# Kernel tuning notes

Measured on AMD Instinct MI355X. Metric: run time of the kernel, lower is better.

Reference implementation:

```python
import jax, jax.numpy as jnp
import numpy as np
import math

B, C_IN, C_OUT, H, W = 16, 128, 128, 56, 56
K, S, P, D = 3, 1, 1, 1
PROD_KS = K * K


def _unfold(x, k, s, p, d):
    # torch.nn.functional.unfold equivalent -> (B, k*k, C, Ho*Wo)
    b, c, h, w = x.shape
    ho = (h + 2 * p - d * (k - 1) - 1) // s + 1
    wo = (w + 2 * p - d * (k - 1) - 1) // s + 1
    xp = jnp.pad(x, ((0, 0), (0, 0), (p, p), (p, p)))
    patches = [
        xp[:, :, i * d: i * d + (ho - 1) * s + 1: s, j * d: j * d + (wo - 1) * s + 1: s]
        for i in range(k) for j in range(k)
    ]
    u = jnp.stack(patches, axis=1)  # (B, K2, C, Ho, Wo)
    return u.reshape(b, k * k, c, ho * wo), ho, wo


def setup_inputs() -> dict:
    key = jax.random.key(0)
    k1, k2, k3, k4 = jax.random.split(key, 4)
    stdv = 1.0 / math.sqrt(C_IN * PROD_KS)
    x = jax.random.normal(k1, (B, C_IN, H, W), dtype=jnp.float32)
    weight = jax.random.uniform(k2, (1, PROD_KS, C_OUT, C_IN), dtype=jnp.float32,
                                minval=-stdv, maxval=stdv)
    b_k = jax.random.uniform(k3, (1, PROD_KS, 1, C_OUT, 1), dtype=jnp.float32,
                             minval=-stdv, maxval=stdv)
    bias = jax.random.uniform(k4, (C_OUT,), dtype=jnp.float32, minval=-stdv, maxval=stdv)
    return {"x": x, "weight": weight, "b_k": b_k, "bias": bias}


def reference(x, weight, b_k, bias):
    batch = x.shape[0]
    u, ho, wo = _unfold(x, K, S, P, D)          # (B, K2, C_in, L)
    inpt = u.transpose(0, 1, 3, 2)               # (B, K2, L, C_in)
    # GEMM: (B,K2,L,Cin) x (K2,Cout,Cin) -> (B,K2,L,Cout)
    out = jnp.einsum('bklc,koc->bklo', inpt, weight[0])
    bk = b_k[0, :, 0, :, 0]                      # (K2, Cout)
    # fused cos/sin contraction over kernel positions -> (B, L, Cout) each
    a = jnp.einsum('bklo,ko->blo', out, jnp.cos(bk))
    bb = jnp.einsum('bklo,ko->blo', out, jnp.sin(bk))
    eps = 1e-05
    a_gt = a > 0
    b_gt = bb > 0
    ab_eq = a_gt == b_gt
    theta = jnp.where(ab_eq, jnp.arctan(bb / (a + eps)), -jnp.arctan(a / (bb + eps)))
    pi = math.pi
    peak = jnp.where(ab_eq & a_gt, pi / 2.0,
           jnp.where(ab_eq & ~a_gt, -pi / 2.0,
           jnp.where(~ab_eq & ~b_gt, -pi, 0.0)))
    theta = peak - theta
    o = jnp.sin(theta) * a + jnp.cos(theta) * bb  # (B, L, Cout)
    o = o.transpose(0, 2, 1) + bias[None, :, None]  # (B, Cout, L)
    conv_out = o.reshape(batch, C_OUT, ho, wo)
    theta_out = (theta / pi).transpose(0, 2, 1).reshape(batch, C_OUT, ho, wo)
    return jnp.concatenate([conv_out, theta_out], axis=1)
```

## Files before the change

### kernel.cpp

```cpp
#include <hip/hip_runtime.h>
#include <hip/hip_bf16.h>
#include <math.h>

#define NB   16
#define CIN  128
#define COUT 128
#define HH   56
#define WW   56
#define LL   3136

typedef __attribute__((ext_vector_type(8))) short short8;
typedef __attribute__((ext_vector_type(16))) float f32x16;
typedef __attribute__((ext_vector_type(4))) float f32x4;
typedef __attribute__((ext_vector_type(4))) unsigned int uint4v;

#define PXT    256
#define NPXT   13
#define XC     58
#define XPLANE 7424
#define XUSH   14848
#define XUNITS 1856
#define XHALF  928
#define WUSH   9216
#define WBYTES 18432
#define WUNITS 1152


#define XT_ROWS 62
#define XT_PLANE_USH (XT_ROWS*XC*16)
#define XT_CG_STRIDE 3682304

#define CSD_OFF 256
#define WSP_OFF 32768
#define XT_OFF  1212416
#define XT_SIZE 29458432
#define WL_OFF  (XT_OFF + XT_SIZE)

__global__ void prep_kernel(const float* __restrict__ w, const float* __restrict__ bk,
                            const float* __restrict__ x,
                            double* __restrict__ csd, unsigned short* __restrict__ wsp,
                            unsigned short* __restrict__ xt, unsigned* __restrict__ cnt) {
    int bid = blockIdx.x;
    if (bid == 0 && threadIdx.x == 0) *cnt = 0u;
    if (bid < 576) {
        int i = bid * 256 + threadIdx.x;
        if (i >= 9*COUT*CIN) return;
        int k = i / (COUT*CIN);
        int rem = i - k*(COUT*CIN);
        int oc = rem >> 7, c = rem & 127;
        float bkv = bk[k*COUT + oc];
        if (c == 0) {
            double bd = (double)bkv;
            csd[k*COUT + oc]          = cos(bd);
            csd[9*COUT + k*COUT + oc] = sin(bd);
        }
        float ck = cosf(bkv), sk = sinf(bkv);
        float wv = w[i];
        float fa = ck * wv;
        float fb = sk * wv;
        __hip_bfloat16 ah = __float2bfloat16(fa);
        __hip_bfloat16 al = __float2bfloat16(fa - __bfloat162float(ah));
        __hip_bfloat16 bh = __float2bfloat16(fb);
        __hip_bfloat16 bl = __float2bfloat16(fb - __bfloat162float(bh));
        int ocb = oc >> 4;
        int row_a = oc & 15;
        int cg = c >> 4, cp = c & 15;
        int lane_a = row_a + ((cp >> 3) << 5);
        int lane_b = 16 + row_a + ((cp >> 3) << 5);
        int bp = cp & 7;
        size_t img = ((size_t)ocb*8 + cg) * WUSH;
        wsp[img + (size_t)((k*2+0)*64 + lane_a)*8 + bp] = *(unsigned short*)&ah;
        wsp[img + (size_t)((k*2+0)*64 + lane_b)*8 + bp] = *(unsigned short*)&bh;
        wsp[img + (size_t)((k*2+1)*64 + lane_a)*8 + bp] = *(unsigned short*)&al;
        wsp[img + (size_t)((k*2+1)*64 + lane_b)*8 + bp] = *(unsigned short*)&bl;
    } else {
        int i = (bid - 576) * 256 + threadIdx.x;
        if (i < 100352) {
            int c4 = i % 14; int t = i / 14;
            int row1 = t % 56; t /= 56;
            int bat = t & 15, cg = t >> 4;
            const float* xp = x + ((size_t)(bat*CIN + cg*16))*LL + row1*WW + c4*4;
            unsigned short hi[4][16], lo[4][16];
            #pragma unroll
            for (int j = 0; j < 16; j++) {
                f32x4 v = *(const f32x4*)(xp + (size_t)j*LL);
                #pragma unroll
                for (int cc = 0; cc < 4; cc++) {
                    float f = v[cc];
                    __hip_bfloat16 h = __float2bfloat16(f);
                    __hip_bfloat16 l = __float2bfloat16(f - __bfloat162float(h));
                    hi[cc][j] = *(unsigned short*)&h;
                    lo[cc][j] = *(unsigned short*)&l;
                }
            }
            size_t base = ((((size_t)cg*16 + bat)*2 + 0)*XT_ROWS + (row1+1))*XC + (c4*4 + 1);
            #pragma unroll
            for (int cc = 0; cc < 4; cc++) {
                unsigned short* dh = xt + (base + cc)*16;
                unsigned short* dl = dh + XT_PLANE_USH;
                *(uint4v*)dh       = *(const uint4v*)&hi[cc][0];
                *(uint4v*)(dh + 8) = *(const uint4v*)&hi[cc][8];
                *(uint4v*)dl       = *(const uint4v*)&lo[cc][0];
                *(uint4v*)(dl + 8) = *(const uint4v*)&lo[cc][8];
            }
        } else if (i < 218112) {
            int i2 = i - 100352;
            int unit = i2 % 460; int t = i2 / 460;
            int pl = t & 1; t >>= 1;
            int bat = t & 15, cg = t >> 4;
            int row, c58;
            if (unit < 348) {
                int zr = unit / 58; c58 = unit - zr*58;
                row = (zr == 0) ? 0 : (56 + zr);
            } else {
                int u2 = unit - 348; row = 1 + (u2 >> 1); c58 = (u2 & 1) ? 57 : 0;
            }
            size_t base = ((((size_t)cg*16 + bat)*2 + pl)*XT_ROWS + row)*XC + c58;
            uint4v zz = {0u,0u,0u,0u};
            *(uint4v*)(xt + base*16)     = zz;
            *(uint4v*)(xt + base*16 + 8) = zz;
        }
    }
}

__global__ __launch_bounds__(256, 3)
void mfma_kernel(const unsigned short* __restrict__ xt, const unsigned short* __restrict__ wsp,
                 const float* __restrict__ bias, float* __restrict__ out,
                 unsigned* __restrict__ cnt, unsigned* __restrict__ wl, unsigned cap)
{
    __shared__ __align__(16) unsigned short SMX[XUSH];
    __shared__ __align__(16) unsigned short SMW[WUSH];
    __shared__ float sm_bias[16];

    const int tid = threadIdx.x;
    int bid = blockIdx.x;
    int wk = (bid & 7) * 208 + (bid >> 3);
    const int ocb = wk & 7; wk >>= 3;
    const int pxt = wk % NPXT;
    const int bat = wk / NPXT;
    const int l0  = pxt * PXT;
    const int o0  = ocb * 16;
    const int yf  = l0 / WW;

    const int lane = tid & 63;
    const int n    = lane & 31;
    const int kh   = lane >> 5;
    const int wave = tid >> 6;

    if (tid < 16) sm_bias[tid] = bias[o0 + tid];

    unsigned xoff[8];
    #pragma unroll
    for (int k = 0; k < 8; k++) {
        int u = tid + 256*k;
        int uc = u < XUNITS ? u : XUNITS-1;
        int pl = uc >= XHALF ? 1 : 0;
        int rem = uc - pl*XHALF;
        int q  = rem >> 1;
        int hl = rem & 1;
        int hg = hl ^ ((q >> 2) & 1);
        int r  = q / XC;
        int c  = q - r*XC;
        xoff[k] = (unsigned)((((bat*2 + pl)*XT_ROWS + (yf + r))*XC + c)*32 + hg*16);
    }

    int q0g[2];
    #pragma unroll
    for (int g = 0; g < 2; g++) {
        int p  = l0 + wave*64 + g*32 + n;
        int pc = p < LL ? p : LL-1;
        int py = pc / WW, pxx = pc - py*WW;
        q0g[g] = (py - yf)*XC + pxx;
    }

    f32x16 acc[2];
    #pragma unroll
    for (int g = 0; g < 2; g++) {
        #pragma unroll
        for (int r = 0; r < 16; r++) acc[g][r] = 0.f;
    }

    const char* xtB  = (const char*)xt;
    const char* wspB = (const char*)wsp + (size_t)ocb * (8*(size_t)WBYTES);

    auto stage_x = [&](int chn) {
        const char* xp = xtB + (size_t)chn * XT_CG_STRIDE;
        #pragma unroll
        for (int k = 0; k < 7; k++) {
            __builtin_amdgcn_global_load_lds(
                (const __attribute__((address_space(1))) unsigned int*)(xp + xoff[k]),
                (__attribute__((address_space(3))) unsigned int*)&SMX[(wave*64 + 256*k)*8],
                16, 0, 0);
        }
        if (wave == 0)
            __builtin_amdgcn_global_load_lds(
                (const __attribute__((address_space(1))) unsigned int*)(xp + xoff[7]),
                (__attribute__((address_space(3))) unsigned int*)&SMX[1792*8],
                16, 0, 0);
    };
    auto stage_w = [&](int chn) {
        const char* wp = wspB + (size_t)chn * (size_t)WBYTES;
        #pragma unroll
        for (int k = 0; k < 4; k++) {
            __builtin_amdgcn_global_load_lds(
                (const __attribute__((address_space(1))) unsigned int*)(wp + (tid + 256*k)*16),
                (__attribute__((address_space(3))) unsigned int*)&SMW[(wave*64 + 256*k)*8],
                16, 0, 0);
        }
        if (wave < 2)
            __builtin_amdgcn_global_load_lds(
                (const __attribute__((address_space(1))) unsigned int*)(wp + (1024 + tid)*16),
                (__attribute__((address_space(3))) unsigned int*)&SMW[(1024 + wave*64)*8],
                16, 0, 0);
    };

    stage_x(0);
    stage_w(0);
    __syncthreads();

    const unsigned short* awp = &SMW[lane*8];

    #pragma unroll 1
    for (int ch = 0; ch < 8; ch++) {
        #pragma unroll
        for (int tap = 0; tap < 9; tap++) {
            const int ky = tap / 3, kx = tap - 3*ky;
            short8 Ah = *(const short8*)&awp[(tap*2+0)*512];
            short8 Al = *(const short8*)&awp[(tap*2+1)*512];
            __builtin_amdgcn_s_setprio(1);
            #pragma unroll
            for (int g = 0; g < 2; g++) {
                int q  = q0g[g] + ky*XC + kx;
                int si = q*16 + ((kh ^ ((q>>2)&1)) << 3);
                short8 Bh = *(const short8*)&SMX[si];
                short8 Bl = *(const short8*)&SMX[XPLANE + si];
                acc[g] = __builtin_amdgcn_mfma_f32_32x32x16_bf16(Al, Bh, acc[g], 0,0,0);
                acc[g] = __builtin_amdgcn_mfma_f32_32x32x16_bf16(Ah, Bl, acc[g], 0,0,0);
                acc[g] = __builtin_amdgcn_mfma_f32_32x32x16_bf16(Ah, Bh, acc[g], 0,0,0);
            }
            __builtin_amdgcn_s_setprio(0);
        }
        if (ch < 7) {
            __syncthreads();
            stage_x(ch+1);
            stage_w(ch+1);
            __syncthreads();
        }
    }

    const float eps = 1e-05f;
    const float PIf = 3.14159265358979323846f;
    size_t obase = (size_t)bat * (2*COUT) * LL;

    #pragma unroll
    for (int g = 0; g < 2; g++) {
        const int pcol = wave*64 + g*32 + n;
        const int pp = l0 + pcol;
        #pragma unroll
        for (int r = 0; r < 8; r++) {
            int row16 = (r & 3) + 8*(r >> 2) + 4*kh;
            float av = acc[g][r];
            float bv = acc[g][r+8];
            bool flag = (pp < LL) &&
                        (fabsf(av) < 1.5e-4f || (bv < 1.05e-5f && bv > -2.05e-5f));
            unsigned long long m = __ballot(flag);
            if (m) {
                int leader = (int)__ffsll((long long)m) - 1;
                unsigned base = 0;
                if (lane == leader) base = atomicAdd(cnt, (unsigned)__popcll(m));
                base = __shfl(base, leader);
                if (flag) {
                    unsigned slot = base + (unsigned)__popcll(m & ((1ULL << lane) - 1ULL));
                    if (slot < cap)
                        wl[slot] = ((unsigned)(bat*LL + pp) << 7) | (unsigned)(o0 + row16);
                }
            }
            bool ag = av > 0.f, bg = bv > 0.f;
            bool eq = (ag == bg);
            float ratio = eq ? (bv / (av + eps)) : (av / (bv + eps));
            float at = atanf(ratio);
            float peak = eq ? (ag ? PIf*0.5f : -PIf*0.5f) : (bg ? 0.0f : -PIf);
            float th = peak - (eq ? at : -at);
            float c = 1.0f / sqrtf(1.0f + ratio*ratio);
            float t = eq ? (av + ratio*bv) : (ratio*av + bv);
            bool pos = eq ? ag : bg;
            float o = (pos ? c : -c) * t;
            if (pp < LL) {
                out[obase + (size_t)(o0+row16)*LL + pp]      = o + sm_bias[row16];
                out[obase + (size_t)(COUT+o0+row16)*LL + pp] = th * (1.0f/PIf);
            }
        }
    }
}

__global__ __launch_bounds__(256)
void fixup_kernel(const float* __restrict__ x, const float* __restrict__ w,
                  const double* __restrict__ csd, const float* __restrict__ bias,
                  const unsigned* __restrict__ cnt, const unsigned* __restrict__ wl,
                  unsigned cap, float* __restrict__ out) {
    const int lane   = threadIdx.x & 63;
    const int waveid = (blockIdx.x * 256 + threadIdx.x) >> 6;
    const int nwaves = gridDim.x * 4;
    unsigned nf = *cnt; if (nf > cap) nf = cap;
    const double PI = 3.14159265358979323846;

    for (unsigned u = waveid; u < nf; u += nwaves) {
        unsigned idx = wl[u];
        int oc = idx & 127;
        unsigned rest = idx >> 7;
        int bb_ = rest / LL;
        int l   = rest - bb_*LL;
        int yy  = l / WW;
        int xx  = l - yy*WW;
        const float* xb = x + (size_t)bb_ * CIN * LL;

        double pa = 0.0, pb = 0.0;
        #pragma unroll
        for (int k = 0; k < 9; k++) {
            int dy = k/3, dx = k - dy*3;
            int py = yy + dy - 1, px = xx + dx - 1;
            double pk = 0.0;
            if ((unsigned)py < HH && (unsigned)px < WW) {
                int base = py*WW + px;
                const float* wr = w + k*(COUT*CIN) + oc*CIN;
                int c = lane;
                pk  = (double)xb[(size_t)c*LL + base] * (double)wr[c];
                c = lane + 64;
                pk += (double)xb[(size_t)c*LL + base] * (double)wr[c];
            }
            pa += csd[k*COUT + oc] * pk;
            pb += csd[9*COUT + k*COUT + oc] * pk;
        }
        #pragma unroll
        for (int off = 32; off > 0; off >>= 1) {
            pa += __shfl_xor(pa, off, 64);
            pb += __shfl_xor(pb, off, 64);
        }
        if (lane == 0) {
            bool ag = pa > 0.0, bg = pb > 0.0;
            bool eq = (ag == bg);
            double th;
            if (eq) th = (ag ? PI*0.5 : -PI*0.5) - atan(pb / (pa + 1e-5));
            else    th = (bg ? 0.0 : -PI) + atan(pa / (pb + 1e-5));
            double o = sin(th)*pa + cos(th)*pb + (double)bias[oc];
            out[((size_t)bb_*(2*COUT) + oc) * LL + l]        = (float)o;
            out[((size_t)bb_*(2*COUT) + COUT + oc) * LL + l] = (float)(th / PI);
        }
    }
}

extern "C" void kernel_launch(void* const* d_in, const int* in_sizes, int n_in,
                              void* d_out, int out_size, void* d_ws, size_t ws_size,
                              hipStream_t stream) {
    const float* x    = (const float*)d_in[0];
    const float* w    = (const float*)d_in[1];
    const float* bk   = (const float*)d_in[2];
    const float* bias = (const float*)d_in[3];
    float* out = (float*)d_out;

    char* ws = (char*)d_ws;
    unsigned*       cnt = (unsigned*)ws;
    double*         csd = (double*)(ws + CSD_OFF);
    unsigned short* wsp = (unsigned short*)(ws + WSP_OFF);
    unsigned short* xt  = (unsigned short*)(ws + XT_OFF);
    unsigned*       wl  = (unsigned*)(ws + WL_OFF);
    unsigned cap = (ws_size > (size_t)WL_OFF + 4096) ? (unsigned)((ws_size - WL_OFF) / 4) : 0u;

    hipLaunchKernelGGL(prep_kernel,  dim3(1428), dim3(256), 0, stream,
                       w, bk, x, csd, wsp, xt, cnt);
    hipLaunchKernelGGL(mfma_kernel,  dim3(NB*NPXT*8), dim3(256), 0, stream,
                       xt, wsp, bias, out, cnt, wl, cap);
    hipLaunchKernelGGL(fixup_kernel, dim3(256), dim3(256), 0, stream,
                       x, w, csd, bias, cnt, wl, cap, out);
}
```

Before: 326.8 us.

## Read activations directly from global memory and double-buffer weights in LDS

Activation tiles are no longer staged into LDS. Each lane now loads its B operands straight from global memory for every tap, and the loads rely on the cache for the 9x reuse across taps. The freed LDS holds double-buffered weights, so the next channel group's weights prefetch while the current one computes, and one barrier per iteration goes away. Launch bounds rise to 4 blocks per CU. The trade-off is many more global loads with long latency inside the MFMA loop, which may stall the compute.

```diff
diff --git a/kernel.cpp b/kernel.cpp
--- a/kernel.cpp
+++ b/kernel.cpp
@@ -17,10 +17,6 @@
 #define PXT    256
 #define NPXT   13
 #define XC     58
-#define XPLANE 7424
-#define XUSH   14848
-#define XUNITS 1856
-#define XHALF  928
 #define WUSH   9216
 #define WBYTES 18432
 #define WUNITS 1152
@@ -28,6 +24,7 @@
 
 #define XT_ROWS 62
 #define XT_PLANE_USH (XT_ROWS*XC*16)
+#define XT_PLANE_B   (XT_ROWS*XC*32)
 #define XT_CG_STRIDE 3682304
 
 #define CSD_OFF 256
@@ -123,13 +120,12 @@
     }
 }
 
-__global__ __launch_bounds__(256, 3)
+__global__ __launch_bounds__(256, 4)
 void mfma_kernel(const unsigned short* __restrict__ xt, const unsigned short* __restrict__ wsp,
                  const float* __restrict__ bias, float* __restrict__ out,
                  unsigned* __restrict__ cnt, unsigned* __restrict__ wl, unsigned cap)
 {
-    __shared__ __align__(16) unsigned short SMX[XUSH];
-    __shared__ __align__(16) unsigned short SMW[WUSH];
+    __shared__ __align__(16) unsigned short SMW[2*WUSH];
     __shared__ float sm_bias[16];
 
     const int tid = threadIdx.x;
@@ -140,7 +136,6 @@
     const int bat = wk / NPXT;
     const int l0  = pxt * PXT;
     const int o0  = ocb * 16;
-    const int yf  = l0 / WW;
 
     const int lane = tid & 63;
     const int n    = lane & 31;
@@ -149,28 +144,15 @@
 
     if (tid < 16) sm_bias[tid] = bias[o0 + tid];
 
-    unsigned xoff[8];
-    #pragma unroll
-    for (int k = 0; k < 8; k++) {
-        int u = tid + 256*k;
-        int uc = u < XUNITS ? u : XUNITS-1;
-        int pl = uc >= XHALF ? 1 : 0;
-        int rem = uc - pl*XHALF;
-        int q  = rem >> 1;
-        int hl = rem & 1;
-        int hg = hl ^ ((q >> 2) & 1);
-        int r  = q / XC;
-        int c  = q - r*XC;
-        xoff[k] = (unsigned)((((bat*2 + pl)*XT_ROWS + (yf + r))*XC + c)*32 + hg*16);
-    }
-
-    int q0g[2];
+    const char* bh[2]; const char* bl[2];
     #pragma unroll
     for (int g = 0; g < 2; g++) {
         int p  = l0 + wave*64 + g*32 + n;
         int pc = p < LL ? p : LL-1;
         int py = pc / WW, pxx = pc - py*WW;
-        q0g[g] = (py - yf)*XC + pxx;
+        size_t off = (((size_t)(bat*2)*XT_ROWS + py)*XC + pxx)*32 + kh*16;
+        bh[g] = (const char*)xt + off;
+        bl[g] = bh[g] + XT_PLANE_B;
     }
 
     f32x16 acc[2];
@@ -180,72 +162,52 @@
         for (int r = 0; r < 16; r++) acc[g][r] = 0.f;
     }
 
-    const char* xtB  = (const char*)xt;
     const char* wspB = (const char*)wsp + (size_t)ocb * (8*(size_t)WBYTES);
 
-    auto stage_x = [&](int chn) {
-        const char* xp = xtB + (size_t)chn * XT_CG_STRIDE;
-        #pragma unroll
-        for (int k = 0; k < 7; k++) {
-            __builtin_amdgcn_global_load_lds(
-                (const __attribute__((address_space(1))) unsigned int*)(xp + xoff[k]),
-                (__attribute__((address_space(3))) unsigned int*)&SMX[(wave*64 + 256*k)*8],
-                16, 0, 0);
-        }
-        if (wave == 0)
-            __builtin_amdgcn_global_load_lds(
-                (const __attribute__((address_space(1))) unsigned int*)(xp + xoff[7]),
-                (__attribute__((address_space(3))) unsigned int*)&SMX[1792*8],
-                16, 0, 0);
-    };
     auto stage_w = [&](int chn) {
         const char* wp = wspB + (size_t)chn * (size_t)WBYTES;
+        unsigned short* dst = &SMW[(chn & 1) * WUSH];
         #pragma unroll
         for (int k = 0; k < 4; k++) {
             __builtin_amdgcn_global_load_lds(
                 (const __attribute__((address_space(1))) unsigned int*)(wp + (tid + 256*k)*16),
-                (__attribute__((address_space(3))) unsigned int*)&SMW[(wave*64 + 256*k)*8],
+                (__attribute__((address_space(3))) unsigned int*)&dst[(wave*64 + 256*k)*8],
                 16, 0, 0);
         }
-        if (wave < 2)
+        if (tid < 128)
             __builtin_amdgcn_global_load_lds(
                 (const __attribute__((address_space(1))) unsigned int*)(wp + (1024 + tid)*16),
-                (__attribute__((address_space(3))) unsigned int*)&SMW[(1024 + wave*64)*8],
+                (__attribute__((address_space(3))) unsigned int*)&SMW[(chn & 1)*WUSH + (1024 + tid)*8],
                 16, 0, 0);
     };
 
-    stage_x(0);
     stage_w(0);
     __syncthreads();
 
-    const unsigned short* awp = &SMW[lane*8];
-
     #pragma unroll 1
     for (int ch = 0; ch < 8; ch++) {
+        if (ch < 7) stage_w(ch+1);
+        const unsigned short* awp = &SMW[(ch & 1) * WUSH + lane*8];
         #pragma unroll
         for (int tap = 0; tap < 9; tap++) {
             const int ky = tap / 3, kx = tap - 3*ky;
+            const int to = (ky*XC + kx)*32;
             short8 Ah = *(const short8*)&awp[(tap*2+0)*512];
             short8 Al = *(const short8*)&awp[(tap*2+1)*512];
             __builtin_amdgcn_s_setprio(1);
             #pragma unroll
             for (int g = 0; g < 2; g++) {
-                int q  = q0g[g] + ky*XC + kx;
-                int si = q*16 + ((kh ^ ((q>>2)&1)) << 3);
-                short8 Bh = *(const short8*)&SMX[si];
-                short8 Bl = *(const short8*)&SMX[XPLANE + si];
+                short8 Bh = *(const short8*)(bh[g] + to);
+                short8 Bl = *(const short8*)(bl[g] + to);
                 acc[g] = __builtin_amdgcn_mfma_f32_32x32x16_bf16(Al, Bh, acc[g], 0,0,0);
                 acc[g] = __builtin_amdgcn_mfma_f32_32x32x16_bf16(Ah, Bl, acc[g], 0,0,0);
                 acc[g] = __builtin_amdgcn_mfma_f32_32x32x16_bf16(Ah, Bh, acc[g], 0,0,0);
             }
             __builtin_amdgcn_s_setprio(0);
         }
-        if (ch < 7) {
-            __syncthreads();
-            stage_x(ch+1);
-            stage_w(ch+1);
-            __syncthreads();
-        }
+        #pragma unroll
+        for (int g = 0; g < 2; g++) { bh[g] += XT_CG_STRIDE; bl[g] += XT_CG_STRIDE; }
+        if (ch < 7) __syncthreads();
     }
 
     const float eps = 1e-05f;
```

After: 330.2 us. Within noise of the previous version (+1.0%).
